# Kernel optimization log

Hardware: AMD Instinct MI355X
Metric: run time of the kernel (lower is better)

Reference implementation:

```python
import jax, jax.numpy as jnp
import numpy as np

N_GENES = 768
HID = 128


def setup_inputs() -> dict:
    key = jax.random.key(0)
    ks = jax.random.split(key, 7)
    s1 = 1.0 / np.sqrt(2 * HID)
    s2 = 1.0 / np.sqrt(HID)
    return {
        "gene_embeddings": jax.random.normal(ks[0], (N_GENES, HID), jnp.float32),
        # regulatory_classifier: Linear(2h -> h), ReLU, Linear(h -> 3)
        "W1": jax.random.normal(ks[1], (HID, 2 * HID), jnp.float32) * s1,
        "b1": jax.random.normal(ks[2], (HID,), jnp.float32) * s1,
        "W2": jax.random.normal(ks[3], (3, HID), jnp.float32) * s2,
        "b2": jax.random.normal(ks[4], (3,), jnp.float32) * s2,
        # binding_predictor: Bilinear(h, h, 1) -> weight [1, h, h], bias [1]
        "Wb": jax.random.normal(ks[5], (1, HID, HID), jnp.float32) * s2,
        "bb": jax.random.normal(ks[6], (1,), jnp.float32) * s2,
    }


def reference(gene_embeddings, W1, b1, W2, b2, Wb, bb):
    """Vectorized equivalent of GeneRegulatoryNetwork.compute_regulatory_matrix.

    For every ordered pair (i, j), i != j:
      logits   = MLP(cat[x_i, x_j])            -> [3]
      cls      = argmax(logits)
      affinity = x_i^T Wb x_j + bb             (nn.Bilinear, out=1)
      reg[i,j] = +affinity if cls==0, -affinity if cls==2, else 0
    """
    X = gene_embeddings  # [n, h]
    n, h = X.shape
    # Linear(2h -> h) on cat[x_i, x_j] splits into two per-gene projections.
    Ai = X @ W1[:, :h].T  # [n, h] contribution of gene_i
    Bj = X @ W1[:, h:].T  # [n, h] contribution of gene_j
    hidden = jax.nn.relu(Ai[:, None, :] + Bj[None, :, :] + b1)  # [n, n, h]
    logits = hidden @ W2.T + b2  # [n, n, 3]
    reg_class = jnp.argmax(logits, axis=-1)  # [n, n] (first-max, matches torch)
    # Bilinear affinity: x_i^T Wb[0] x_j + bb[0]
    affinity = jnp.einsum('ik,kl,jl->ij', X, Wb[0], X) + bb[0]  # [n, n]
    sign = jnp.where(reg_class == 0, 1.0, jnp.where(reg_class == 2, -1.0, 0.0))
    reg = (sign * affinity).astype(X.dtype)
    # i == j pairs are skipped in the original loop -> zero diagonal
    reg = reg * (1.0 - jnp.eye(n, dtype=reg.dtype))
    return reg
```

## Files before the change

kernel.cpp:

```cpp
#include <hip/hip_runtime.h>

#define N_GENES 768
#define H 128
#define TILE 48
#define LDP 132
#define LDPH 136

typedef float    f2 __attribute__((ext_vector_type(2)));
typedef _Float16 h2 __attribute__((ext_vector_type(2)));
typedef _Float16 h8 __attribute__((ext_vector_type(8)));

__global__ __launch_bounds__(128) void grn_pre(
    const float* __restrict__ X, const float* __restrict__ W1,
    const float* __restrict__ b1, const float* __restrict__ Wb,
    float* __restrict__ AiB, float* __restrict__ Bjp,
    _Float16* __restrict__ Yh, _Float16* __restrict__ Xh)
{
    const int m  = threadIdx.x;
    const int g0 = blockIdx.x * 3;

    __shared__ float Xs[3][H];
    #pragma unroll
    for (int r = 0; r < 3; ++r) Xs[r][m] = X[(g0 + r) * H + m];
    __syncthreads();

    double aib[3] = {0, 0, 0}, bj[3] = {0, 0, 0}, y[3] = {0, 0, 0};
    const float4* W1a = (const float4*)(W1 + m * (2 * H));
    const float4* W1b = (const float4*)(W1 + m * (2 * H) + H);

    #pragma unroll 4
    for (int kq = 0; kq < H / 4; ++kq) {
        float4 wa = W1a[kq];
        float4 wb = W1b[kq];
        float wc[4];
        #pragma unroll
        for (int e = 0; e < 4; ++e) wc[e] = Wb[(kq * 4 + e) * H + m];
        const float* wae = &wa.x;
        const float* wbe = &wb.x;
        #pragma unroll
        for (int r = 0; r < 3; ++r) {
            float4 xr = *(const float4*)&Xs[r][kq * 4];
            const float* xe = &xr.x;
            #pragma unroll
            for (int e = 0; e < 4; ++e) {
                aib[r] += (double)xe[e] * (double)wae[e];
                bj[r]  += (double)xe[e] * (double)wbe[e];
                y[r]   += (double)xe[e] * (double)wc[e];
            }
        }
    }

    const double b1m = (double)b1[m];
    #pragma unroll
    for (int r = 0; r < 3; ++r) {
        AiB[(g0 + r) * H + m] = (float)(aib[r] + b1m);
        Bjp[(g0 + r) * H + m] = (float)bj[r];
        Yh [(g0 + r) * H + m] = (_Float16)(float)y[r];
        Xh [(g0 + r) * H + m] = (_Float16)Xs[r][m];
    }
}

__device__ __forceinline__ void load_tile_f32(float* __restrict__ dst,
                                              const float* __restrict__ src, int tx)
{
    #pragma unroll
    for (int t = 0; t < 6; ++t) {
        int idx = tx + t * 256;
        int row = idx >> 5;
        int c4  = idx & 31;
        *(float4*)&dst[row * LDP + c4 * 4] = *(const float4*)&src[row * H + c4 * 4];
    }
}

__device__ __forceinline__ void load_tile_f16(_Float16* __restrict__ dst,
                                              const _Float16* __restrict__ src, int tx)
{
    #pragma unroll
    for (int t = 0; t < 3; ++t) {
        int idx = tx + t * 256;
        int row = idx >> 4;
        int c8  = idx & 15;
        *(h8*)&dst[row * LDPH + c8 * 8] = *(const h8*)&src[row * H + c8 * 8];
    }
}

__device__ __forceinline__ h2 hpair(h8 v, int p) { h2 r; r.x = v[2*p]; r.y = v[2*p+1]; return r; }

__global__ __launch_bounds__(256) void grn_main(
    const float* __restrict__ AiB, const float* __restrict__ Bjp,
    const _Float16* __restrict__ Yh, const _Float16* __restrict__ Xh,
    const float* __restrict__ W2,  const float* __restrict__ b2,
    const float* __restrict__ bb,  float* __restrict__ out)
{
    const int gj = blockIdx.x & 15;
    const int gi = blockIdx.x >> 4;
    const int tx = threadIdx.x;
    const int it = tx >> 4;
    const int jt = tx & 15;

    __shared__ float sL[TILE * LDP];
    __shared__ float sR[TILE * LDP];
    __shared__ float sW[2 * H];

    _Float16* sLh = (_Float16*)sL;
    _Float16* sRh = (_Float16*)sR;

    load_tile_f16(sLh, Yh + gi * TILE * H, tx);
    load_tile_f16(sRh, Xh + gj * TILE * H, tx);
    if (tx < H) {
        sW[tx]     = W2[tx] - W2[2 * H + tx];
        sW[H + tx] = W2[tx] - W2[H + tx];
    }
    __syncthreads();

    float aff[3][3] = {};
    #pragma unroll 2
    for (int q = 0; q < H / 8; ++q) {
        h8 yv[3], xv[3];
        #pragma unroll
        for (int r = 0; r < 3; ++r) yv[r] = *(const h8*)&sLh[(it + 16 * r) * LDPH + q * 8];
        #pragma unroll
        for (int c = 0; c < 3; ++c) xv[c] = *(const h8*)&sRh[(jt + 16 * c) * LDPH + q * 8];
        #pragma unroll
        for (int r = 0; r < 3; ++r)
            #pragma unroll
            for (int c = 0; c < 3; ++c)
                #pragma unroll
                for (int p = 0; p < 4; ++p) {
#if __has_builtin(__builtin_amdgcn_fdot2)
                    aff[r][c] = __builtin_amdgcn_fdot2(hpair(yv[r], p), hpair(xv[c], p),
                                                       aff[r][c], false);
#else
                    h2 a = hpair(yv[r], p), b = hpair(xv[c], p);
                    aff[r][c] = fmaf((float)a.x, (float)b.x, aff[r][c]);
                    aff[r][c] = fmaf((float)a.y, (float)b.y, aff[r][c]);
#endif
                }
    }

    __syncthreads();

    load_tile_f32(sL, AiB + gi * TILE * H, tx);
    load_tile_f32(sR, Bjp + gj * TILE * H, tx);
    __syncthreads();

    const float u0 = b2[0] - b2[2];
    const float v0 = b2[0] - b2[1];
    float u[3][3], v[3][3];
    #pragma unroll
    for (int r = 0; r < 3; ++r)
        #pragma unroll
        for (int c = 0; c < 3; ++c) { u[r][c] = u0; v[r][c] = v0; }

    const f2 zero2 = {0.0f, 0.0f};
    #pragma unroll 4
    for (int mq = 0; mq < H / 4; ++mq) {
        float4 w0 = *(const float4*)&sW[mq * 4];
        float4 w1 = *(const float4*)&sW[H + mq * 4];
        float4 av[3], bv[3];
        #pragma unroll
        for (int r = 0; r < 3; ++r) av[r] = *(const float4*)&sL[(it + 16 * r) * LDP + mq * 4];
        #pragma unroll
        for (int c = 0; c < 3; ++c) bv[c] = *(const float4*)&sR[(jt + 16 * c) * LDP + mq * 4];
        #pragma unroll
        for (int r = 0; r < 3; ++r) {
            f2 a01 = {av[r].x, av[r].y};
            f2 a23 = {av[r].z, av[r].w};
            #pragma unroll
            for (int c = 0; c < 3; ++c) {
                f2 b01 = {bv[c].x, bv[c].y};
                f2 b23 = {bv[c].z, bv[c].w};
                f2 h01 = __builtin_elementwise_max(a01 + b01, zero2);
                f2 h23 = __builtin_elementwise_max(a23 + b23, zero2);
                float uu = u[r][c], vv = v[r][c];
                uu = fmaf(h01.x, w0.x, uu); vv = fmaf(h01.x, w1.x, vv);
                uu = fmaf(h01.y, w0.y, uu); vv = fmaf(h01.y, w1.y, vv);
                uu = fmaf(h23.x, w0.z, uu); vv = fmaf(h23.x, w1.z, vv);
                uu = fmaf(h23.y, w0.w, uu); vv = fmaf(h23.y, w1.w, vv);
                u[r][c] = uu; v[r][c] = vv;
            }
        }
    }

    const float bbv = bb[0];
    #pragma unroll
    for (int r = 0; r < 3; ++r) {
        const int i = gi * TILE + it + 16 * r;
        #pragma unroll
        for (int c = 0; c < 3; ++c) {
            const int j = gj * TILE + jt + 16 * c;
            float A = aff[r][c] + bbv;
            float uu = u[r][c], vv = v[r][c];
            float s = (uu >= 0.0f && vv >= 0.0f) ? A
                    : ((uu < 0.0f && uu < vv) ? -A : 0.0f);
            if (i == j) s = 0.0f;
            out[i * N_GENES + j] = s;
        }
    }
}

extern "C" void kernel_launch(void* const* d_in, const int* in_sizes, int n_in,
                              void* d_out, int out_size, void* d_ws, size_t ws_size,
                              hipStream_t stream)
{
    const float* X  = (const float*)d_in[0];
    const float* W1 = (const float*)d_in[1];
    const float* b1 = (const float*)d_in[2];
    const float* W2 = (const float*)d_in[3];
    const float* b2 = (const float*)d_in[4];
    const float* Wb = (const float*)d_in[5];
    const float* bb = (const float*)d_in[6];
    float* out = (float*)d_out;

    float* ws  = (float*)d_ws;
    float*     AiB = ws;
    float*     Bjp = ws + N_GENES * H;
    _Float16*  Yh  = (_Float16*)(ws + 2 * N_GENES * H);
    _Float16*  Xh  = (_Float16*)(ws + 2 * N_GENES * H) + N_GENES * H;

    grn_pre <<<N_GENES / 3, 128, 0, stream>>>(X, W1, b1, Wb, AiB, Bjp, Yh, Xh);
    grn_main<<<256,         256, 0, stream>>>(AiB, Bjp, Yh, Xh, W2, b2, bb, out);
}
```

Baseline: 88.33 us.

## Compute bilinear affinity with MFMA and precompute W2 differences in pre kernel

The bilinear affinity tile is now computed with 16x16x32 f16 MFMA instructions reading directly from global memory, and the results are staged through a shared-memory buffer, replacing the per-thread fdot2 loop and the separate f16 tile load. The W2 difference vectors move into the pre-kernel and are read from global memory inside the main loop instead of from shared memory. The pre-kernel now handles 2 genes per block and accumulates Y in float rather than double. This removes a synchronisation phase and scalar dot work, but adds uncoalesced global loads and a lower-precision Y accumulation that could flip near-zero signs.

```diff
diff --git a/kernel.cpp b/kernel.cpp
--- a/kernel.cpp
+++ b/kernel.cpp
@@ -4,27 +4,29 @@
 #define H 128
 #define TILE 48
 #define LDP 132
-#define LDPH 136
-
-typedef float    f2 __attribute__((ext_vector_type(2)));
-typedef _Float16 h2 __attribute__((ext_vector_type(2)));
-typedef _Float16 h8 __attribute__((ext_vector_type(8)));
+#define AFFP 49
+
+typedef float    f2    __attribute__((ext_vector_type(2)));
+typedef float    f32x4 __attribute__((ext_vector_type(4)));
+typedef _Float16 h8    __attribute__((ext_vector_type(8)));
 
 __global__ __launch_bounds__(128) void grn_pre(
     const float* __restrict__ X, const float* __restrict__ W1,
     const float* __restrict__ b1, const float* __restrict__ Wb,
-    float* __restrict__ AiB, float* __restrict__ Bjp,
+    const float* __restrict__ W2,
+    float* __restrict__ AiB, float* __restrict__ Bjp, float* __restrict__ Wd,
     _Float16* __restrict__ Yh, _Float16* __restrict__ Xh)
 {
     const int m  = threadIdx.x;
-    const int g0 = blockIdx.x * 3;
-
-    __shared__ float Xs[3][H];
-    #pragma unroll
-    for (int r = 0; r < 3; ++r) Xs[r][m] = X[(g0 + r) * H + m];
+    const int g0 = blockIdx.x * 2;
+
+    __shared__ float Xs[2][H];
+    #pragma unroll
+    for (int r = 0; r < 2; ++r) Xs[r][m] = X[(g0 + r) * H + m];
     __syncthreads();
 
-    double aib[3] = {0, 0, 0}, bj[3] = {0, 0, 0}, y[3] = {0, 0, 0};
+    double aib[2] = {0, 0}, bj[2] = {0, 0};
+    float  y[2]   = {0.0f, 0.0f};
     const float4* W1a = (const float4*)(W1 + m * (2 * H));
     const float4* W1b = (const float4*)(W1 + m * (2 * H) + H);
 
@@ -38,25 +40,30 @@
         const float* wae = &wa.x;
         const float* wbe = &wb.x;
         #pragma unroll
-        for (int r = 0; r < 3; ++r) {
+        for (int r = 0; r < 2; ++r) {
             float4 xr = *(const float4*)&Xs[r][kq * 4];
             const float* xe = &xr.x;
             #pragma unroll
             for (int e = 0; e < 4; ++e) {
                 aib[r] += (double)xe[e] * (double)wae[e];
                 bj[r]  += (double)xe[e] * (double)wbe[e];
-                y[r]   += (double)xe[e] * (double)wc[e];
+                y[r]    = fmaf(xe[e], wc[e], y[r]);
             }
         }
     }
 
     const double b1m = (double)b1[m];
     #pragma unroll
-    for (int r = 0; r < 3; ++r) {
+    for (int r = 0; r < 2; ++r) {
         AiB[(g0 + r) * H + m] = (float)(aib[r] + b1m);
         Bjp[(g0 + r) * H + m] = (float)bj[r];
-        Yh [(g0 + r) * H + m] = (_Float16)(float)y[r];
+        Yh [(g0 + r) * H + m] = (_Float16)y[r];
         Xh [(g0 + r) * H + m] = (_Float16)Xs[r][m];
+    }
+
+    if (blockIdx.x == 0) {
+        Wd[m]     = W2[m] - W2[2 * H + m];
+        Wd[H + m] = W2[m] - W2[H + m];
     }
 }
 
@@ -72,24 +79,10 @@
     }
 }
 
-__device__ __forceinline__ void load_tile_f16(_Float16* __restrict__ dst,
-                                              const _Float16* __restrict__ src, int tx)
-{
-    #pragma unroll
-    for (int t = 0; t < 3; ++t) {
-        int idx = tx + t * 256;
-        int row = idx >> 4;
-        int c8  = idx & 15;
-        *(h8*)&dst[row * LDPH + c8 * 8] = *(const h8*)&src[row * H + c8 * 8];
-    }
-}
-
-__device__ __forceinline__ h2 hpair(h8 v, int p) { h2 r; r.x = v[2*p]; r.y = v[2*p+1]; return r; }
-
 __global__ __launch_bounds__(256) void grn_main(
     const float* __restrict__ AiB, const float* __restrict__ Bjp,
     const _Float16* __restrict__ Yh, const _Float16* __restrict__ Xh,
-    const float* __restrict__ W2,  const float* __restrict__ b2,
+    const float* __restrict__ Wd,  const float* __restrict__ b2,
     const float* __restrict__ bb,  float* __restrict__ out)
 {
     const int gj = blockIdx.x & 15;
@@ -100,48 +93,31 @@
 
     __shared__ float sL[TILE * LDP];
     __shared__ float sR[TILE * LDP];
-    __shared__ float sW[2 * H];
-
-    _Float16* sLh = (_Float16*)sL;
-    _Float16* sRh = (_Float16*)sR;
-
-    load_tile_f16(sLh, Yh + gi * TILE * H, tx);
-    load_tile_f16(sRh, Xh + gj * TILE * H, tx);
-    if (tx < H) {
-        sW[tx]     = W2[tx] - W2[2 * H + tx];
-        sW[H + tx] = W2[tx] - W2[H + tx];
-    }
-    __syncthreads();
-
-    float aff[3][3] = {};
-    #pragma unroll 2
-    for (int q = 0; q < H / 8; ++q) {
-        h8 yv[3], xv[3];
-        #pragma unroll
-        for (int r = 0; r < 3; ++r) yv[r] = *(const h8*)&sLh[(it + 16 * r) * LDPH + q * 8];
-        #pragma unroll
-        for (int c = 0; c < 3; ++c) xv[c] = *(const h8*)&sRh[(jt + 16 * c) * LDPH + q * 8];
-        #pragma unroll
-        for (int r = 0; r < 3; ++r)
-            #pragma unroll
-            for (int c = 0; c < 3; ++c)
-                #pragma unroll
-                for (int p = 0; p < 4; ++p) {
-#if __has_builtin(__builtin_amdgcn_fdot2)
-                    aff[r][c] = __builtin_amdgcn_fdot2(hpair(yv[r], p), hpair(xv[c], p),
-                                                       aff[r][c], false);
-#else
-                    h2 a = hpair(yv[r], p), b = hpair(xv[c], p);
-                    aff[r][c] = fmaf((float)a.x, (float)b.x, aff[r][c]);
-                    aff[r][c] = fmaf((float)a.y, (float)b.y, aff[r][c]);
-#endif
-                }
-    }
-
-    __syncthreads();
+    __shared__ float affS[TILE * AFFP];
 
     load_tile_f32(sL, AiB + gi * TILE * H, tx);
     load_tile_f32(sR, Bjp + gj * TILE * H, tx);
+
+    {
+        const int lane = tx & 63;
+        const int wv   = tx >> 6;
+        const int lrow = lane & 15;
+        const int lq   = lane >> 4;
+        for (int t = wv; t < 9; t += 4) {
+            const int tr = t / 3, tc = t % 3;
+            const _Float16* ya = Yh + (gi * TILE + tr * 16 + lrow) * H + lq * 8;
+            const _Float16* xb = Xh + (gj * TILE + tc * 16 + lrow) * H + lq * 8;
+            f32x4 a = {0.0f, 0.0f, 0.0f, 0.0f};
+            #pragma unroll
+            for (int k0 = 0; k0 < 4; ++k0)
+                a = __builtin_amdgcn_mfma_f32_16x16x32_f16(
+                        *(const h8*)(ya + k0 * 32), *(const h8*)(xb + k0 * 32), a, 0, 0, 0);
+            #pragma unroll
+            for (int j = 0; j < 4; ++j)
+                affS[(tr * 16 + lq * 4 + j) * AFFP + tc * 16 + lrow] = a[j];
+        }
+    }
+
     __syncthreads();
 
     const float u0 = b2[0] - b2[2];
@@ -153,10 +129,11 @@
         for (int c = 0; c < 3; ++c) { u[r][c] = u0; v[r][c] = v0; }
 
     const f2 zero2 = {0.0f, 0.0f};
+    const float4* Wd4 = (const float4*)Wd;
     #pragma unroll 4
     for (int mq = 0; mq < H / 4; ++mq) {
-        float4 w0 = *(const float4*)&sW[mq * 4];
-        float4 w1 = *(const float4*)&sW[H + mq * 4];
+        float4 w0 = Wd4[mq];
+        float4 w1 = Wd4[32 + mq];
         float4 av[3], bv[3];
         #pragma unroll
         for (int r = 0; r < 3; ++r) av[r] = *(const float4*)&sL[(it + 16 * r) * LDP + mq * 4];
@@ -189,7 +166,7 @@
         #pragma unroll
         for (int c = 0; c < 3; ++c) {
             const int j = gj * TILE + jt + 16 * c;
-            float A = aff[r][c] + bbv;
+            float A = affS[(it + 16 * r) * AFFP + (jt + 16 * c)] + bbv;
             float uu = u[r][c], vv = v[r][c];
             float s = (uu >= 0.0f && vv >= 0.0f) ? A
                     : ((uu < 0.0f && uu < vv) ? -A : 0.0f);
@@ -212,12 +189,13 @@
     const float* bb = (const float*)d_in[6];
     float* out = (float*)d_out;
 
-    float* ws  = (float*)d_ws;
-    float*     AiB = ws;
-    float*     Bjp = ws + N_GENES * H;
-    _Float16*  Yh  = (_Float16*)(ws + 2 * N_GENES * H);
-    _Float16*  Xh  = (_Float16*)(ws + 2 * N_GENES * H) + N_GENES * H;
-
-    grn_pre <<<N_GENES / 3, 128, 0, stream>>>(X, W1, b1, Wb, AiB, Bjp, Yh, Xh);
-    grn_main<<<256,         256, 0, stream>>>(AiB, Bjp, Yh, Xh, W2, b2, bb, out);
-}
+    float* ws = (float*)d_ws;
+    float*    AiB = ws;
+    float*    Bjp = ws + N_GENES * H;
+    float*    Wd  = ws + 2 * N_GENES * H;
+    _Float16* Yh  = (_Float16*)(ws + 2 * N_GENES * H + 256);
+    _Float16* Xh  = Yh + N_GENES * H;
+
+    grn_pre <<<N_GENES / 2, 128, 0, stream>>>(X, W1, b1, Wb, W2, AiB, Bjp, Wd, Yh, Xh);
+    grn_main<<<256,         256, 0, stream>>>(AiB, Bjp, Yh, Xh, Wd, b2, bb, out);
+}
```

Result: slower. 104.7 us (+18.5%).

## Read Ai rows and W2 diffs from global, pack u/v into float2 FMAs

Applied to the files above, without the earlier changes.

The precomputed W2 row differences move into the pre kernel and are stored interleaved in the workspace. The main kernel no longer stages the AiB tile in shared memory. Each thread reads its three Ai rows and the interleaved weights straight from global (likely cache-resident), which removes two barriers and lets the Bj tile load together with the f16 tiles. The u/v accumulators become a float2 so the compiler can emit packed FMAs. The trade-off is more global/L1 traffic in the inner loop in exchange for less LDS use and fewer synchronisations.

```diff
diff --git a/kernel.cpp b/kernel.cpp
--- a/kernel.cpp
+++ b/kernel.cpp
@@ -13,7 +13,8 @@
 __global__ __launch_bounds__(128) void grn_pre(
     const float* __restrict__ X, const float* __restrict__ W1,
     const float* __restrict__ b1, const float* __restrict__ Wb,
-    float* __restrict__ AiB, float* __restrict__ Bjp,
+    const float* __restrict__ W2,
+    float* __restrict__ AiB, float* __restrict__ Bjp, float* __restrict__ Wd,
     _Float16* __restrict__ Yh, _Float16* __restrict__ Xh)
 {
     const int m  = threadIdx.x;
@@ -58,6 +59,11 @@
         Yh [(g0 + r) * H + m] = (_Float16)(float)y[r];
         Xh [(g0 + r) * H + m] = (_Float16)Xs[r][m];
     }
+
+    if (blockIdx.x == 0) {
+        Wd[2 * m]     = W2[m] - W2[2 * H + m];
+        Wd[2 * m + 1] = W2[m] - W2[H + m];
+    }
 }
 
 __device__ __forceinline__ void load_tile_f32(float* __restrict__ dst,
@@ -89,7 +95,7 @@
 __global__ __launch_bounds__(256) void grn_main(
     const float* __restrict__ AiB, const float* __restrict__ Bjp,
     const _Float16* __restrict__ Yh, const _Float16* __restrict__ Xh,
-    const float* __restrict__ W2,  const float* __restrict__ b2,
+    const float* __restrict__ Wd,  const float* __restrict__ b2,
     const float* __restrict__ bb,  float* __restrict__ out)
 {
     const int gj = blockIdx.x & 15;
@@ -98,19 +104,13 @@
     const int it = tx >> 4;
     const int jt = tx & 15;
 
-    __shared__ float sL[TILE * LDP];
-    __shared__ float sR[TILE * LDP];
-    __shared__ float sW[2 * H];
-
-    _Float16* sLh = (_Float16*)sL;
-    _Float16* sRh = (_Float16*)sR;
+    __shared__ _Float16 sLh[TILE * LDPH];
+    __shared__ _Float16 sRh[TILE * LDPH];
+    __shared__ float    sR [TILE * LDP];
 
     load_tile_f16(sLh, Yh + gi * TILE * H, tx);
     load_tile_f16(sRh, Xh + gj * TILE * H, tx);
-    if (tx < H) {
-        sW[tx]     = W2[tx] - W2[2 * H + tx];
-        sW[H + tx] = W2[tx] - W2[H + tx];
-    }
+    load_tile_f32(sR,  Bjp + gj * TILE * H, tx);
     __syncthreads();
 
     float aff[3][3] = {};
@@ -138,28 +138,24 @@
                 }
     }
 
-    __syncthreads();
-
-    load_tile_f32(sL, AiB + gi * TILE * H, tx);
-    load_tile_f32(sR, Bjp + gj * TILE * H, tx);
-    __syncthreads();
-
-    const float u0 = b2[0] - b2[2];
-    const float v0 = b2[0] - b2[1];
-    float u[3][3], v[3][3];
+    const f2 uv0 = {b2[0] - b2[2], b2[0] - b2[1]};
+    f2 uv[3][3];
     #pragma unroll
     for (int r = 0; r < 3; ++r)
         #pragma unroll
-        for (int c = 0; c < 3; ++c) { u[r][c] = u0; v[r][c] = v0; }
+        for (int c = 0; c < 3; ++c) uv[r][c] = uv0;
+
+    const float* aRow = AiB + (gi * TILE + it) * H;
+    const float4* Wduv = (const float4*)Wd;
 
     const f2 zero2 = {0.0f, 0.0f};
     #pragma unroll 4
     for (int mq = 0; mq < H / 4; ++mq) {
-        float4 w0 = *(const float4*)&sW[mq * 4];
-        float4 w1 = *(const float4*)&sW[H + mq * 4];
+        float4 wq0 = Wduv[2 * mq];
+        float4 wq1 = Wduv[2 * mq + 1];
         float4 av[3], bv[3];
         #pragma unroll
-        for (int r = 0; r < 3; ++r) av[r] = *(const float4*)&sL[(it + 16 * r) * LDP + mq * 4];
+        for (int r = 0; r < 3; ++r) av[r] = *(const float4*)(aRow + r * 16 * H + mq * 4);
         #pragma unroll
         for (int c = 0; c < 3; ++c) bv[c] = *(const float4*)&sR[(jt + 16 * c) * LDP + mq * 4];
         #pragma unroll
@@ -172,12 +168,12 @@
                 f2 b23 = {bv[c].z, bv[c].w};
                 f2 h01 = __builtin_elementwise_max(a01 + b01, zero2);
                 f2 h23 = __builtin_elementwise_max(a23 + b23, zero2);
-                float uu = u[r][c], vv = v[r][c];
-                uu = fmaf(h01.x, w0.x, uu); vv = fmaf(h01.x, w1.x, vv);
-                uu = fmaf(h01.y, w0.y, uu); vv = fmaf(h01.y, w1.y, vv);
-                uu = fmaf(h23.x, w0.z, uu); vv = fmaf(h23.x, w1.z, vv);
-                uu = fmaf(h23.y, w0.w, uu); vv = fmaf(h23.y, w1.w, vv);
-                u[r][c] = uu; v[r][c] = vv;
+                f2 t = uv[r][c];
+                t = (f2){h01.x, h01.x} * (f2){wq0.x, wq0.y} + t;
+                t = (f2){h01.y, h01.y} * (f2){wq0.z, wq0.w} + t;
+                t = (f2){h23.x, h23.x} * (f2){wq1.x, wq1.y} + t;
+                t = (f2){h23.y, h23.y} * (f2){wq1.z, wq1.w} + t;
+                uv[r][c] = t;
             }
         }
     }
@@ -190,7 +186,7 @@
         for (int c = 0; c < 3; ++c) {
             const int j = gj * TILE + jt + 16 * c;
             float A = aff[r][c] + bbv;
-            float uu = u[r][c], vv = v[r][c];
+            float uu = uv[r][c].x, vv = uv[r][c].y;
             float s = (uu >= 0.0f && vv >= 0.0f) ? A
                     : ((uu < 0.0f && uu < vv) ? -A : 0.0f);
             if (i == j) s = 0.0f;
@@ -212,12 +208,13 @@
     const float* bb = (const float*)d_in[6];
     float* out = (float*)d_out;
 
-    float* ws  = (float*)d_ws;
-    float*     AiB = ws;
-    float*     Bjp = ws + N_GENES * H;
-    _Float16*  Yh  = (_Float16*)(ws + 2 * N_GENES * H);
-    _Float16*  Xh  = (_Float16*)(ws + 2 * N_GENES * H) + N_GENES * H;
-
-    grn_pre <<<N_GENES / 3, 128, 0, stream>>>(X, W1, b1, Wb, AiB, Bjp, Yh, Xh);
-    grn_main<<<256,         256, 0, stream>>>(AiB, Bjp, Yh, Xh, W2, b2, bb, out);
-}
+    float* ws = (float*)d_ws;
+    float*    AiB = ws;
+    float*    Bjp = ws + N_GENES * H;
+    float*    Wd  = ws + 2 * N_GENES * H;
+    _Float16* Yh  = (_Float16*)(ws + 2 * N_GENES * H + 256);
+    _Float16* Xh  = Yh + N_GENES * H;
+
+    grn_pre <<<N_GENES / 3, 128, 0, stream>>>(X, W1, b1, Wb, W2, AiB, Bjp, Wd, Yh, Xh);
+    grn_main<<<256,         256, 0, stream>>>(AiB, Bjp, Yh, Xh, Wd, b2, bb, out);
+}
```

After: 90.45 us. 1.02x slower.
